# Performance work log

Measured on AMD Instinct MI355X. Metric: run time of the kernel, lower is better.

## Reference

```python
import jax, jax.numpy as jnp
import numpy as np

N = 100000
E = 3200000
IN = 128
HID = 128   # 2 * out_channels
OUT = 64


def setup_inputs() -> dict:
    key = jax.random.key(0)
    ks = jax.random.split(key, 8)
    x = jax.random.normal(ks[0], (N, IN), dtype=jnp.float32)
    edge_index = jax.random.randint(ks[1], (2, E), 0, N, dtype=jnp.int64)
    s1 = 1.0 / np.sqrt(IN)
    s2 = 1.0 / np.sqrt(HID)
    # PyG GraphConv per layer: lin_rel (with bias) applied to aggregated neighbors,
    # lin_root (no bias) applied to the node itself. Linear weight is (out, in).
    W1_rel = jax.random.uniform(ks[2], (HID, IN), jnp.float32, -s1, s1)
    b1 = jax.random.uniform(ks[3], (HID,), jnp.float32, -s1, s1)
    W1_root = jax.random.uniform(ks[4], (HID, IN), jnp.float32, -s1, s1)
    W2_rel = jax.random.uniform(ks[5], (OUT, HID), jnp.float32, -s2, s2)
    b2 = jax.random.uniform(ks[6], (OUT,), jnp.float32, -s2, s2)
    W2_root = jax.random.uniform(ks[7], (OUT, HID), jnp.float32, -s2, s2)
    return {"x": x, "edge_index": edge_index, "W1_rel": W1_rel, "b1": b1,
            "W1_root": W1_root, "W2_rel": W2_rel, "b2": b2, "W2_root": W2_root}


def _graph_conv(h, src, dst, W_rel, b, W_root, num_nodes):
    # sum-aggregate neighbor features at dst, then affine combine with root term
    agg = jax.ops.segment_sum(h[src], dst, num_segments=num_nodes)  # [N, d_in]
    return agg @ W_rel.T + b + h @ W_root.T


def reference(x, edge_index, W1_rel, b1, W1_root, W2_rel, b2, W2_root):
    src = edge_index[0]
    dst = edge_index[1]
    n = x.shape[0]
    h = _graph_conv(x, src, dst, W1_rel, b1, W1_root, n)
    h = jax.nn.relu(h)  # dropout p=0.0 -> identity
    return _graph_conv(h, src, dst, W2_rel, b2, W2_root, n)
```

## Files before the change

kernel.cpp:

```cpp
#include <hip/hip_runtime.h>
#include <hip/hip_bf16.h>


#define EB 8192
#define NB_MAX 512

typedef __attribute__((ext_vector_type(8))) short bf16x8;
typedef __attribute__((ext_vector_type(4))) float f32x4;
typedef __attribute__((ext_vector_type(2))) float f32x2;

__device__ __forceinline__ uint pack_bf16x2(float a, float b) {
    __hip_bfloat162 p = __float22bfloat162_rn(make_float2(a, b));
    return *(uint*)&p;
}

__device__ __forceinline__ uchar pack_fp8(float v) {
    uint p = __builtin_amdgcn_cvt_pk_fp8_f32(v, v, 0, false);
    return (uchar)(p & 0xff);
}

__device__ __forceinline__ float bflo(uint g) { return __uint_as_float(g << 16); }
__device__ __forceinline__ float bfhi(uint g) { return __uint_as_float(g & 0xffff0000u); }


__global__ __launch_bounds__(256) void bucket_hist(const int* __restrict__ dst, int E,
                                                   int NB, int* __restrict__ hist) {
    __shared__ int h[NB_MAX];
    int t = threadIdx.x;
    for (int i = t; i < NB; i += 256) h[i] = 0;
    __syncthreads();
    int e0 = blockIdx.x * EB, e1 = min(E, e0 + EB);
    for (int e = e0 + t; e < e1; e += 256) atomicAdd(&h[dst[e] >> 8], 1);
    __syncthreads();
    int* row = hist + (size_t)blockIdx.x * NB;
    for (int i = t; i < NB; i += 256) row[i] = h[i];
}

__global__ __launch_bounds__(256) void scan_blocks(int* __restrict__ hist, int NBLK,
                                                   int NB, int* __restrict__ total) {
    __shared__ int s[256];
    __shared__ int carry;
    int b = blockIdx.x, t = threadIdx.x;
    if (t == 0) carry = 0;
    __syncthreads();
    for (int start = 0; start < NBLK; start += 256) {
        int i = start + t;
        int v = (i < NBLK) ? hist[(size_t)i * NB + b] : 0;
        s[t] = v;
        __syncthreads();
        for (int off = 1; off < 256; off <<= 1) {
            int u = (t >= off) ? s[t - off] : 0;
            __syncthreads();
            s[t] += u;
            __syncthreads();
        }
        if (i < NBLK) hist[(size_t)i * NB + b] = carry + s[t] - v;
        __syncthreads();
        if (t == 255) carry += s[255];
        __syncthreads();
    }
    if (t == 0) total[b] = carry;
}

__global__ __launch_bounds__(512) void scan_total(const int* __restrict__ total, int NB,
                                                  int* __restrict__ base) {
    __shared__ int s[512];
    int t = threadIdx.x;
    int v = (t < NB) ? total[t] : 0;
    s[t] = v;
    __syncthreads();
    for (int off = 1; off < 512; off <<= 1) {
        int u = (t >= off) ? s[t - off] : 0;
        __syncthreads();
        s[t] += u;
        __syncthreads();
    }
    if (t < NB) base[t] = s[t] - v;
}

__global__ __launch_bounds__(256) void bucket_scatter(const int* __restrict__ src,
                                                      const int* __restrict__ dst, int E,
                                                      int NB, const int* __restrict__ hist,
                                                      const int* __restrict__ base,
                                                      uint* __restrict__ ebuf) {
    __shared__ int cur[NB_MAX];
    int t = threadIdx.x, blk = blockIdx.x;
    const int* row = hist + (size_t)blk * NB;
    for (int i = t; i < NB; i += 256) cur[i] = base[i] + row[i];
    __syncthreads();
    int e0 = blk * EB, e1 = min(E, e0 + EB);
    for (int e = e0 + t; e < e1; e += 256) {
        int d = dst[e];
        int p = atomicAdd(&cur[d >> 8], 1);
        ebuf[p] = ((uint)(d & 255) << 24) | (uint)src[e];
    }
}

__global__ __launch_bounds__(256) void build_csr_bucket(const uint* __restrict__ ebuf,
                                                        const int* __restrict__ base,
                                                        const int* __restrict__ total,
                                                        int NB, int N, int E,
                                                        int* __restrict__ rowptr,
                                                        int* __restrict__ col) {
    __shared__ int cnt[256];
    __shared__ int s[256];
    __shared__ int cur[256];
    int b = blockIdx.x, t = threadIdx.x;
    int e0 = base[b], e1 = e0 + total[b];
    cnt[t] = 0;
    __syncthreads();
    for (int e = e0 + t; e < e1; e += 256) atomicAdd(&cnt[ebuf[e] >> 24], 1);
    __syncthreads();
    int v = cnt[t];
    s[t] = v;
    __syncthreads();
    for (int off = 1; off < 256; off <<= 1) {
        int u = (t >= off) ? s[t - off] : 0;
        __syncthreads();
        s[t] += u;
        __syncthreads();
    }
    int start = e0 + s[t] - v;
    int node = (b << 8) + t;
    if (node < N) rowptr[node] = start;
    if (b == NB - 1 && t == 0) rowptr[N] = E;
    cur[t] = start;
    __syncthreads();
    for (int e = e0 + t; e < e1; e += 256) {
        uint ev = ebuf[e];
        int p = atomicAdd(&cur[ev >> 24], 1);
        col[p] = (int)(ev & 0xFFFFFFu);
    }
}


#define LDK 72

template <int C, bool A_BF16, bool Y_FP8>
__global__ __launch_bounds__(256, 2) void gemm_mfma(const void* __restrict__ Aptr,
                                                    const float* __restrict__ Wa,
                                                    const float* __restrict__ Wb,
                                                    const float* __restrict__ bias,
                                                    void* __restrict__ Yout,
                                                    float* __restrict__ Z, int n_rows) {
    __shared__ ushort Xs[128 * LDK];
    __shared__ ushort Ws[128 * LDK];

    const int t = threadIdx.x;
    const int lane = t & 63;
    const int wave = t >> 6;
    const int wm = wave >> 1, wn = wave & 1;
    const int row0 = blockIdx.x * 128;
    const int tn = blockIdx.y;
    const int fr = lane & 15;
    const int quad = lane >> 4;

    f32x4 acc[4][4];
#pragma unroll
    for (int i = 0; i < 4; i++)
#pragma unroll
        for (int j = 0; j < 4; j++) acc[i][j] = (f32x4){0.f, 0.f, 0.f, 0.f};

    for (int ko = 0; ko < 2; ++ko) {
        if (A_BF16) {
            const ushort* A = (const ushort*)Aptr;
#pragma unroll
            for (int j = 0; j < 4; ++j) {
                int f = j * 256 + t;
                int r = f >> 3, c = f & 7;
                int grow = row0 + r;
                uint4 v = make_uint4(0u, 0u, 0u, 0u);
                if (grow < n_rows)
                    v = *(const uint4*)(A + (size_t)grow * 128 + ko * 64 + c * 8);
                *(uint4*)(&Xs[r * LDK + c * 8]) = v;
            }
        } else {
            const float* A = (const float*)Aptr;
#pragma unroll
            for (int j = 0; j < 8; ++j) {
                int f = j * 256 + t;
                int r = f >> 4, c = f & 15;
                int grow = row0 + r;
                float4 v = make_float4(0.f, 0.f, 0.f, 0.f);
                if (grow < n_rows)
                    v = *(const float4*)(A + (size_t)grow * 128 + ko * 64 + c * 4);
                uint2 u;
                u.x = pack_bf16x2(v.x, v.y);
                u.y = pack_bf16x2(v.z, v.w);
                *(uint2*)(&Xs[r * LDK + c * 4]) = u;
            }
        }
#pragma unroll
        for (int j = 0; j < 8; ++j) {
            int f = j * 256 + t;
            int r = f >> 4, c = f & 15;
            int grow = tn * 128 + r;
            const float* Wr = (grow < C) ? (Wa + (size_t)grow * 128)
                                         : (Wb + (size_t)(grow - C) * 128);
            float4 v = *(const float4*)(Wr + ko * 64 + c * 4);
            uint2 u;
            u.x = pack_bf16x2(v.x, v.y);
            u.y = pack_bf16x2(v.z, v.w);
            *(uint2*)(&Ws[r * LDK + c * 4]) = u;
        }
        __syncthreads();

#pragma unroll
        for (int ks = 0; ks < 2; ++ks) {
            bf16x8 a[4], b[4];
#pragma unroll
            for (int mt = 0; mt < 4; ++mt)
                a[mt] = *(const bf16x8*)(&Xs[(wm * 64 + mt * 16 + fr) * LDK +
                                             ks * 32 + quad * 8]);
#pragma unroll
            for (int nt = 0; nt < 4; ++nt)
                b[nt] = *(const bf16x8*)(&Ws[(wn * 64 + nt * 16 + fr) * LDK +
                                             ks * 32 + quad * 8]);
#pragma unroll
            for (int mt = 0; mt < 4; ++mt)
#pragma unroll
                for (int nt = 0; nt < 4; ++nt)
                    acc[mt][nt] = __builtin_amdgcn_mfma_f32_16x16x32_bf16(
                        a[mt], b[nt], acc[mt][nt], 0, 0, 0);
        }
        __syncthreads();
    }

#pragma unroll
    for (int nt = 0; nt < 4; ++nt) {
        int gcol = tn * 128 + wn * 64 + nt * 16 + fr;
        if (gcol < C) {
#pragma unroll
            for (int mt = 0; mt < 4; ++mt) {
#pragma unroll
                for (int r = 0; r < 4; ++r) {
                    int grow = row0 + wm * 64 + mt * 16 + quad * 4 + r;
                    if (grow < n_rows) {
                        if (Y_FP8) {
                            ((uchar*)Yout)[(size_t)grow * C + gcol] =
                                pack_fp8(acc[mt][nt][r]);
                        } else {
                            __hip_bfloat16 hb = __float2bfloat16(acc[mt][nt][r]);
                            ((ushort*)Yout)[(size_t)grow * C + gcol] = *(ushort*)&hb;
                        }
                    }
                }
            }
        } else {
            float bv = bias[gcol - C];
#pragma unroll
            for (int mt = 0; mt < 4; ++mt) {
#pragma unroll
                for (int r = 0; r < 4; ++r) {
                    int grow = row0 + wm * 64 + mt * 16 + quad * 4 + r;
                    if (grow < n_rows)
                        Z[(size_t)grow * C + (gcol - C)] = acc[mt][nt][r] + bv;
                }
            }
        }
    }
}


__global__ __launch_bounds__(256) void agg_relu_l1(const uchar* __restrict__ Y1,
                                                   const float* __restrict__ Z1,
                                                   const int* __restrict__ rowptr,
                                                   const int* __restrict__ col,
                                                   ushort* __restrict__ h, int n_nodes) {
    int node = (blockIdx.x * 256 + threadIdx.x) >> 6;
    if (node >= n_nodes) return;
    int lane = threadIdx.x & 63;
    int sub = lane >> 3;
    int cg  = lane & 7;
    int beg = rowptr[node], end = rowptr[node + 1];
    float acc[16];
#pragma unroll
    for (int i = 0; i < 16; i++) acc[i] = 0.f;

    int e = beg;
    for (; e + 16 <= end; e += 16) {
        int s0 = col[e + sub];
        int s1 = col[e + 8 + sub];
        uint4 v0 = *(const uint4*)(Y1 + (size_t)s0 * 128 + cg * 16);
        uint4 v1 = *(const uint4*)(Y1 + (size_t)s1 * 128 + cg * 16);
        f32x2 p;
        p = __builtin_amdgcn_cvt_pk_f32_fp8(v0.x, false); acc[0] += p[0]; acc[1] += p[1];
        p = __builtin_amdgcn_cvt_pk_f32_fp8(v0.x, true);  acc[2] += p[0]; acc[3] += p[1];
        p = __builtin_amdgcn_cvt_pk_f32_fp8(v0.y, false); acc[4] += p[0]; acc[5] += p[1];
        p = __builtin_amdgcn_cvt_pk_f32_fp8(v0.y, true);  acc[6] += p[0]; acc[7] += p[1];
        p = __builtin_amdgcn_cvt_pk_f32_fp8(v0.z, false); acc[8] += p[0]; acc[9] += p[1];
        p = __builtin_amdgcn_cvt_pk_f32_fp8(v0.z, true);  acc[10] += p[0]; acc[11] += p[1];
        p = __builtin_amdgcn_cvt_pk_f32_fp8(v0.w, false); acc[12] += p[0]; acc[13] += p[1];
        p = __builtin_amdgcn_cvt_pk_f32_fp8(v0.w, true);  acc[14] += p[0]; acc[15] += p[1];
        p = __builtin_amdgcn_cvt_pk_f32_fp8(v1.x, false); acc[0] += p[0]; acc[1] += p[1];
        p = __builtin_amdgcn_cvt_pk_f32_fp8(v1.x, true);  acc[2] += p[0]; acc[3] += p[1];
        p = __builtin_amdgcn_cvt_pk_f32_fp8(v1.y, false); acc[4] += p[0]; acc[5] += p[1];
        p = __builtin_amdgcn_cvt_pk_f32_fp8(v1.y, true);  acc[6] += p[0]; acc[7] += p[1];
        p = __builtin_amdgcn_cvt_pk_f32_fp8(v1.z, false); acc[8] += p[0]; acc[9] += p[1];
        p = __builtin_amdgcn_cvt_pk_f32_fp8(v1.z, true);  acc[10] += p[0]; acc[11] += p[1];
        p = __builtin_amdgcn_cvt_pk_f32_fp8(v1.w, false); acc[12] += p[0]; acc[13] += p[1];
        p = __builtin_amdgcn_cvt_pk_f32_fp8(v1.w, true);  acc[14] += p[0]; acc[15] += p[1];
    }
    for (; e < end; e += 8) {
        int ee = e + sub;
        uint4 v = make_uint4(0u, 0u, 0u, 0u);
        if (ee < end)
            v = *(const uint4*)(Y1 + (size_t)col[ee] * 128 + cg * 16);
        f32x2 p;
        p = __builtin_amdgcn_cvt_pk_f32_fp8(v.x, false); acc[0] += p[0]; acc[1] += p[1];
        p = __builtin_amdgcn_cvt_pk_f32_fp8(v.x, true);  acc[2] += p[0]; acc[3] += p[1];
        p = __builtin_amdgcn_cvt_pk_f32_fp8(v.y, false); acc[4] += p[0]; acc[5] += p[1];
        p = __builtin_amdgcn_cvt_pk_f32_fp8(v.y, true);  acc[6] += p[0]; acc[7] += p[1];
        p = __builtin_amdgcn_cvt_pk_f32_fp8(v.z, false); acc[8] += p[0]; acc[9] += p[1];
        p = __builtin_amdgcn_cvt_pk_f32_fp8(v.z, true);  acc[10] += p[0]; acc[11] += p[1];
        p = __builtin_amdgcn_cvt_pk_f32_fp8(v.w, false); acc[12] += p[0]; acc[13] += p[1];
        p = __builtin_amdgcn_cvt_pk_f32_fp8(v.w, true);  acc[14] += p[0]; acc[15] += p[1];
    }

#pragma unroll
    for (int off = 8; off < 64; off <<= 1)
#pragma unroll
        for (int i = 0; i < 16; i++) acc[i] += __shfl_xor(acc[i], off, 64);

    if (sub == 0) {
        const float4* zp = (const float4*)(Z1 + (size_t)node * 128 + cg * 16);
        uint o[8];
#pragma unroll
        for (int q = 0; q < 4; ++q) {
            float4 z = zp[q];
            float r0 = acc[q * 4 + 0] + z.x;
            float r1 = acc[q * 4 + 1] + z.y;
            float r2 = acc[q * 4 + 2] + z.z;
            float r3 = acc[q * 4 + 3] + z.w;
            r0 = r0 > 0.f ? r0 : 0.f;
            r1 = r1 > 0.f ? r1 : 0.f;
            r2 = r2 > 0.f ? r2 : 0.f;
            r3 = r3 > 0.f ? r3 : 0.f;
            o[q * 2 + 0] = pack_bf16x2(r0, r1);
            o[q * 2 + 1] = pack_bf16x2(r2, r3);
        }
        uint* hp = (uint*)(h + (size_t)node * 128) + cg * 8;
        *(uint4*)(hp + 0) = make_uint4(o[0], o[1], o[2], o[3]);
        *(uint4*)(hp + 4) = make_uint4(o[4], o[5], o[6], o[7]);
    }
}


__global__ __launch_bounds__(256) void agg_l2(const ushort* __restrict__ Y2,
                                              const float* __restrict__ Z2,
                                              const int* __restrict__ rowptr,
                                              const int* __restrict__ col,
                                              float* __restrict__ out, int n_nodes) {
    int node = (blockIdx.x * 256 + threadIdx.x) >> 6;
    if (node >= n_nodes) return;
    int lane = threadIdx.x & 63;
    int sub = lane >> 3;
    int cg  = lane & 7;
    int beg = rowptr[node], end = rowptr[node + 1];
    float acc[8];
#pragma unroll
    for (int i = 0; i < 8; i++) acc[i] = 0.f;

    int e = beg;
    for (; e + 16 <= end; e += 16) {
        int s0 = col[e + sub];
        int s1 = col[e + 8 + sub];
        uint4 v0 = *(const uint4*)(Y2 + (size_t)s0 * 64 + cg * 8);
        uint4 v1 = *(const uint4*)(Y2 + (size_t)s1 * 64 + cg * 8);
        acc[0] += bflo(v0.x) + bflo(v1.x);
        acc[1] += bfhi(v0.x) + bfhi(v1.x);
        acc[2] += bflo(v0.y) + bflo(v1.y);
        acc[3] += bfhi(v0.y) + bfhi(v1.y);
        acc[4] += bflo(v0.z) + bflo(v1.z);
        acc[5] += bfhi(v0.z) + bfhi(v1.z);
        acc[6] += bflo(v0.w) + bflo(v1.w);
        acc[7] += bfhi(v0.w) + bfhi(v1.w);
    }
    for (; e < end; e += 8) {
        int ee = e + sub;
        uint4 v = make_uint4(0u, 0u, 0u, 0u);
        if (ee < end)
            v = *(const uint4*)(Y2 + (size_t)col[ee] * 64 + cg * 8);
        acc[0] += bflo(v.x);
        acc[1] += bfhi(v.x);
        acc[2] += bflo(v.y);
        acc[3] += bfhi(v.y);
        acc[4] += bflo(v.z);
        acc[5] += bfhi(v.z);
        acc[6] += bflo(v.w);
        acc[7] += bfhi(v.w);
    }

#pragma unroll
    for (int off = 8; off < 64; off <<= 1)
#pragma unroll
        for (int i = 0; i < 8; i++) acc[i] += __shfl_xor(acc[i], off, 64);

    if (sub == 0) {
        const float4* zp = (const float4*)(Z2 + (size_t)node * 64 + cg * 8);
        float4 z0 = zp[0], z1 = zp[1];
        float4 o0 = {acc[0] + z0.x, acc[1] + z0.y, acc[2] + z0.z, acc[3] + z0.w};
        float4 o1 = {acc[4] + z1.x, acc[5] + z1.y, acc[6] + z1.z, acc[7] + z1.w};
        float4* op = (float4*)(out + (size_t)node * 64 + cg * 8);
        op[0] = o0;
        op[1] = o1;
    }
}


extern "C" void kernel_launch(void* const* d_in, const int* in_sizes, int n_in,
                              void* d_out, int out_size, void* d_ws, size_t ws_size,
                              hipStream_t stream) {
    const float* x       = (const float*)d_in[0];
    const int*   ei      = (const int*)d_in[1];
    const float* W1_rel  = (const float*)d_in[2];
    const float* b1      = (const float*)d_in[3];
    const float* W1_root = (const float*)d_in[4];
    const float* W2_rel  = (const float*)d_in[5];
    const float* b2      = (const float*)d_in[6];
    const float* W2_root = (const float*)d_in[7];
    float* out = (float*)d_out;

    const int N = in_sizes[0] / 128;
    const int E = in_sizes[1] / 2;
    const int* srcA = ei;
    const int* dstA = ei + E;
    const int NB   = (N + 255) >> 8;
    const int NBLK = (E + EB - 1) / EB;

    char* ws = (char*)d_ws;
    size_t cur = 0;
    auto alloc = [&](size_t bytes) -> void* {
        size_t o = cur;
        cur = (cur + bytes + 511) & ~(size_t)511;
        return (void*)(ws + o);
    };
    uchar*  Y1  = (uchar*)alloc((size_t)N * 128);
    float*  Z1  = (float*)alloc((size_t)N * 128 * 4);
    ushort* h   = (ushort*)alloc((size_t)N * 128 * 2);
    ushort* Y2  = (ushort*)alloc((size_t)N * 64 * 2);
    float*  Z2  = (float*)alloc((size_t)N * 64 * 4);
    int* rowptr = (int*)alloc((size_t)(N + 1) * 4);
    int* colA   = (int*)alloc((size_t)E * 4);
    int* hist   = (int*)alloc((size_t)NBLK * NB * 4);
    int* btotal = (int*)alloc((size_t)NB_MAX * 4);
    int* bbase  = (int*)alloc((size_t)NB_MAX * 4);
    uint* ebuf  = (uint*)h;

    bucket_hist<<<NBLK, 256, 0, stream>>>(dstA, E, NB, hist);
    scan_blocks<<<NB, 256, 0, stream>>>(hist, NBLK, NB, btotal);
    scan_total<<<1, 512, 0, stream>>>(btotal, NB, bbase);
    bucket_scatter<<<NBLK, 256, 0, stream>>>(srcA, dstA, E, NB, hist, bbase, ebuf);
    build_csr_bucket<<<NB, 256, 0, stream>>>(ebuf, bbase, btotal, NB, N, E, rowptr, colA);

    const int gblk = (N + 127) / 128;
    gemm_mfma<128, false, true><<<dim3(gblk, 2), 256, 0, stream>>>(
        x, W1_rel, W1_root, b1, Y1, Z1, N);
    agg_relu_l1<<<(N + 3) / 4, 256, 0, stream>>>(Y1, Z1, rowptr, colA, h, N);
    gemm_mfma<64, true, false><<<dim3(gblk, 1), 256, 0, stream>>>(
        h, W2_rel, W2_root, b2, Y2, Z2, N);
    agg_l2<<<(N + 3) / 4, 256, 0, stream>>>(Y2, Z2, rowptr, colA, out, N);
}
```

Before: 426.1 us.

## Pre-convert weights to bf16, load GEMM operands directly, unroll gather loops

Adds a small kernel that converts both layers' weights to bf16 once per call. The GEMMs now read their A and B fragments straight from global memory into registers, with no LDS staging or barriers, and occupancy is raised to 3 blocks. The aggregation kernels process 32 edges per iteration and accumulate into packed float2 vectors. Dropping LDS gives up data reuse across waves, so each wave issues more redundant global and L2 loads. The deeper unroll aims for more memory-level parallelism in the gathers.

```diff
diff --git a/kernel.cpp b/kernel.cpp
--- a/kernel.cpp
+++ b/kernel.cpp
@@ -134,18 +134,43 @@
 }
 
 
-#define LDK 72
+__global__ __launch_bounds__(256) void prep_w(const float* __restrict__ W1_rel,
+                                              const float* __restrict__ W1_root,
+                                              const float* __restrict__ W2_rel,
+                                              const float* __restrict__ W2_root,
+                                              ushort* __restrict__ Wb1,
+                                              ushort* __restrict__ Wb2) {
+    int t = blockIdx.x * 256 + threadIdx.x;
+    if (t < 8192) {
+        int idx = t * 4;
+        int row = idx >> 7, c = idx & 127;
+        const float* src = (row < 128) ? W1_rel + (size_t)row * 128 + c
+                                       : W1_root + (size_t)(row - 128) * 128 + c;
+        float4 v = *(const float4*)src;
+        uint2 u;
+        u.x = pack_bf16x2(v.x, v.y);
+        u.y = pack_bf16x2(v.z, v.w);
+        *(uint2*)(Wb1 + idx) = u;
+    } else if (t < 12288) {
+        int idx = (t - 8192) * 4;
+        int row = idx >> 7, c = idx & 127;
+        const float* src = (row < 64) ? W2_rel + (size_t)row * 128 + c
+                                      : W2_root + (size_t)(row - 64) * 128 + c;
+        float4 v = *(const float4*)src;
+        uint2 u;
+        u.x = pack_bf16x2(v.x, v.y);
+        u.y = pack_bf16x2(v.z, v.w);
+        *(uint2*)(Wb2 + idx) = u;
+    }
+}
+
 
 template <int C, bool A_BF16, bool Y_FP8>
-__global__ __launch_bounds__(256, 2) void gemm_mfma(const void* __restrict__ Aptr,
-                                                    const float* __restrict__ Wa,
-                                                    const float* __restrict__ Wb,
-                                                    const float* __restrict__ bias,
-                                                    void* __restrict__ Yout,
-                                                    float* __restrict__ Z, int n_rows) {
-    __shared__ ushort Xs[128 * LDK];
-    __shared__ ushort Ws[128 * LDK];
-
+__global__ __launch_bounds__(256, 3) void gemm_direct(const void* __restrict__ Aptr,
+                                                      const ushort* __restrict__ Wb16,
+                                                      const float* __restrict__ bias,
+                                                      void* __restrict__ Yout,
+                                                      float* __restrict__ Z, int n_rows) {
     const int t = threadIdx.x;
     const int lane = t & 63;
     const int wave = t >> 6;
@@ -161,69 +186,43 @@
 #pragma unroll
         for (int j = 0; j < 4; j++) acc[i][j] = (f32x4){0.f, 0.f, 0.f, 0.f};
 
-    for (int ko = 0; ko < 2; ++ko) {
-        if (A_BF16) {
-            const ushort* A = (const ushort*)Aptr;
-#pragma unroll
-            for (int j = 0; j < 4; ++j) {
-                int f = j * 256 + t;
-                int r = f >> 3, c = f & 7;
-                int grow = row0 + r;
-                uint4 v = make_uint4(0u, 0u, 0u, 0u);
-                if (grow < n_rows)
-                    v = *(const uint4*)(A + (size_t)grow * 128 + ko * 64 + c * 8);
-                *(uint4*)(&Xs[r * LDK + c * 8]) = v;
+    int ar[4];
+#pragma unroll
+    for (int mt = 0; mt < 4; ++mt) {
+        int r = row0 + wm * 64 + mt * 16 + fr;
+        ar[mt] = (r < n_rows) ? r : (n_rows - 1);
+    }
+    const int brbase = tn * 128 + wn * 64;
+
+#pragma unroll
+    for (int kk = 0; kk < 4; ++kk) {
+        const int kb = kk * 32 + quad * 8;
+        bf16x8 a[4], b[4];
+#pragma unroll
+        for (int mt = 0; mt < 4; ++mt) {
+            if (A_BF16) {
+                a[mt] = *(const bf16x8*)((const ushort*)Aptr + (size_t)ar[mt] * 128 + kb);
+            } else {
+                const float* p = (const float*)Aptr + (size_t)ar[mt] * 128 + kb;
+                float4 v0 = *(const float4*)p;
+                float4 v1 = *(const float4*)(p + 4);
+                uint4 u;
+                u.x = pack_bf16x2(v0.x, v0.y);
+                u.y = pack_bf16x2(v0.z, v0.w);
+                u.z = pack_bf16x2(v1.x, v1.y);
+                u.w = pack_bf16x2(v1.z, v1.w);
+                a[mt] = *(bf16x8*)&u;
             }
-        } else {
-            const float* A = (const float*)Aptr;
-#pragma unroll
-            for (int j = 0; j < 8; ++j) {
-                int f = j * 256 + t;
-                int r = f >> 4, c = f & 15;
-                int grow = row0 + r;
-                float4 v = make_float4(0.f, 0.f, 0.f, 0.f);
-                if (grow < n_rows)
-                    v = *(const float4*)(A + (size_t)grow * 128 + ko * 64 + c * 4);
-                uint2 u;
-                u.x = pack_bf16x2(v.x, v.y);
-                u.y = pack_bf16x2(v.z, v.w);
-                *(uint2*)(&Xs[r * LDK + c * 4]) = u;
-            }
-        }
-#pragma unroll
-        for (int j = 0; j < 8; ++j) {
-            int f = j * 256 + t;
-            int r = f >> 4, c = f & 15;
-            int grow = tn * 128 + r;
-            const float* Wr = (grow < C) ? (Wa + (size_t)grow * 128)
-                                         : (Wb + (size_t)(grow - C) * 128);
-            float4 v = *(const float4*)(Wr + ko * 64 + c * 4);
-            uint2 u;
-            u.x = pack_bf16x2(v.x, v.y);
-            u.y = pack_bf16x2(v.z, v.w);
-            *(uint2*)(&Ws[r * LDK + c * 4]) = u;
-        }
-        __syncthreads();
-
-#pragma unroll
-        for (int ks = 0; ks < 2; ++ks) {
-            bf16x8 a[4], b[4];
-#pragma unroll
-            for (int mt = 0; mt < 4; ++mt)
-                a[mt] = *(const bf16x8*)(&Xs[(wm * 64 + mt * 16 + fr) * LDK +
-                                             ks * 32 + quad * 8]);
+        }
+#pragma unroll
+        for (int nt = 0; nt < 4; ++nt)
+            b[nt] = *(const bf16x8*)(Wb16 + (size_t)(brbase + nt * 16 + fr) * 128 + kb);
+#pragma unroll
+        for (int mt = 0; mt < 4; ++mt)
 #pragma unroll
             for (int nt = 0; nt < 4; ++nt)
-                b[nt] = *(const bf16x8*)(&Ws[(wn * 64 + nt * 16 + fr) * LDK +
-                                             ks * 32 + quad * 8]);
-#pragma unroll
-            for (int mt = 0; mt < 4; ++mt)
-#pragma unroll
-                for (int nt = 0; nt < 4; ++nt)
-                    acc[mt][nt] = __builtin_amdgcn_mfma_f32_16x16x32_bf16(
-                        a[mt], b[nt], acc[mt][nt], 0, 0, 0);
-        }
-        __syncthreads();
+                acc[mt][nt] = __builtin_amdgcn_mfma_f32_16x16x32_bf16(
+                    a[mt], b[nt], acc[mt][nt], 0, 0, 0);
     }
 
 #pragma unroll
@@ -262,6 +261,19 @@
 }
 
 
+#define ACC_FP8(v)                                                           \
+    {                                                                        \
+        f32x2 p;                                                             \
+        p = __builtin_amdgcn_cvt_pk_f32_fp8((v).x, false); acc2[0] += p;     \
+        p = __builtin_amdgcn_cvt_pk_f32_fp8((v).x, true);  acc2[1] += p;     \
+        p = __builtin_amdgcn_cvt_pk_f32_fp8((v).y, false); acc2[2] += p;     \
+        p = __builtin_amdgcn_cvt_pk_f32_fp8((v).y, true);  acc2[3] += p;     \
+        p = __builtin_amdgcn_cvt_pk_f32_fp8((v).z, false); acc2[4] += p;     \
+        p = __builtin_amdgcn_cvt_pk_f32_fp8((v).z, true);  acc2[5] += p;     \
+        p = __builtin_amdgcn_cvt_pk_f32_fp8((v).w, false); acc2[6] += p;     \
+        p = __builtin_amdgcn_cvt_pk_f32_fp8((v).w, true);  acc2[7] += p;     \
+    }
+
 __global__ __launch_bounds__(256) void agg_relu_l1(const uchar* __restrict__ Y1,
                                                    const float* __restrict__ Z1,
                                                    const int* __restrict__ rowptr,
@@ -273,54 +285,50 @@
     int sub = lane >> 3;
     int cg  = lane & 7;
     int beg = rowptr[node], end = rowptr[node + 1];
-    float acc[16];
-#pragma unroll
-    for (int i = 0; i < 16; i++) acc[i] = 0.f;
+    f32x2 acc2[8];
+#pragma unroll
+    for (int i = 0; i < 8; i++) acc2[i] = (f32x2){0.f, 0.f};
 
     int e = beg;
+    for (; e + 32 <= end; e += 32) {
+        int s0 = col[e + sub];
+        int s1 = col[e + 8 + sub];
+        int s2 = col[e + 16 + sub];
+        int s3 = col[e + 24 + sub];
+        uint4 v0 = *(const uint4*)(Y1 + (size_t)s0 * 128 + cg * 16);
+        uint4 v1 = *(const uint4*)(Y1 + (size_t)s1 * 128 + cg * 16);
+        uint4 v2 = *(const uint4*)(Y1 + (size_t)s2 * 128 + cg * 16);
+        uint4 v3 = *(const uint4*)(Y1 + (size_t)s3 * 128 + cg * 16);
+        ACC_FP8(v0);
+        ACC_FP8(v1);
+        ACC_FP8(v2);
+        ACC_FP8(v3);
+    }
     for (; e + 16 <= end; e += 16) {
         int s0 = col[e + sub];
         int s1 = col[e + 8 + sub];
         uint4 v0 = *(const uint4*)(Y1 + (size_t)s0 * 128 + cg * 16);
         uint4 v1 = *(const uint4*)(Y1 + (size_t)s1 * 128 + cg * 16);
-        f32x2 p;
-        p = __builtin_amdgcn_cvt_pk_f32_fp8(v0.x, false); acc[0] += p[0]; acc[1] += p[1];
-        p = __builtin_amdgcn_cvt_pk_f32_fp8(v0.x, true);  acc[2] += p[0]; acc[3] += p[1];
-        p = __builtin_amdgcn_cvt_pk_f32_fp8(v0.y, false); acc[4] += p[0]; acc[5] += p[1];
-        p = __builtin_amdgcn_cvt_pk_f32_fp8(v0.y, true);  acc[6] += p[0]; acc[7] += p[1];
-        p = __builtin_amdgcn_cvt_pk_f32_fp8(v0.z, false); acc[8] += p[0]; acc[9] += p[1];
-        p = __builtin_amdgcn_cvt_pk_f32_fp8(v0.z, true);  acc[10] += p[0]; acc[11] += p[1];
-        p = __builtin_amdgcn_cvt_pk_f32_fp8(v0.w, false); acc[12] += p[0]; acc[13] += p[1];
-        p = __builtin_amdgcn_cvt_pk_f32_fp8(v0.w, true);  acc[14] += p[0]; acc[15] += p[1];
-        p = __builtin_amdgcn_cvt_pk_f32_fp8(v1.x, false); acc[0] += p[0]; acc[1] += p[1];
-        p = __builtin_amdgcn_cvt_pk_f32_fp8(v1.x, true);  acc[2] += p[0]; acc[3] += p[1];
-        p = __builtin_amdgcn_cvt_pk_f32_fp8(v1.y, false); acc[4] += p[0]; acc[5] += p[1];
-        p = __builtin_amdgcn_cvt_pk_f32_fp8(v1.y, true);  acc[6] += p[0]; acc[7] += p[1];
-        p = __builtin_amdgcn_cvt_pk_f32_fp8(v1.z, false); acc[8] += p[0]; acc[9] += p[1];
-        p = __builtin_amdgcn_cvt_pk_f32_fp8(v1.z, true);  acc[10] += p[0]; acc[11] += p[1];
-        p = __builtin_amdgcn_cvt_pk_f32_fp8(v1.w, false); acc[12] += p[0]; acc[13] += p[1];
-        p = __builtin_amdgcn_cvt_pk_f32_fp8(v1.w, true);  acc[14] += p[0]; acc[15] += p[1];
+        ACC_FP8(v0);
+        ACC_FP8(v1);
     }
     for (; e < end; e += 8) {
         int ee = e + sub;
         uint4 v = make_uint4(0u, 0u, 0u, 0u);
         if (ee < end)
             v = *(const uint4*)(Y1 + (size_t)col[ee] * 128 + cg * 16);
-        f32x2 p;
-        p = __builtin_amdgcn_cvt_pk_f32_fp8(v.x, false); acc[0] += p[0]; acc[1] += p[1];
-        p = __builtin_amdgcn_cvt_pk_f32_fp8(v.x, true);  acc[2] += p[0]; acc[3] += p[1];
-        p = __builtin_amdgcn_cvt_pk_f32_fp8(v.y, false); acc[4] += p[0]; acc[5] += p[1];
-        p = __builtin_amdgcn_cvt_pk_f32_fp8(v.y, true);  acc[6] += p[0]; acc[7] += p[1];
-        p = __builtin_amdgcn_cvt_pk_f32_fp8(v.z, false); acc[8] += p[0]; acc[9] += p[1];
-        p = __builtin_amdgcn_cvt_pk_f32_fp8(v.z, true);  acc[10] += p[0]; acc[11] += p[1];
-        p = __builtin_amdgcn_cvt_pk_f32_fp8(v.w, false); acc[12] += p[0]; acc[13] += p[1];
-        p = __builtin_amdgcn_cvt_pk_f32_fp8(v.w, true);  acc[14] += p[0]; acc[15] += p[1];
+        ACC_FP8(v);
     }
 
 #pragma unroll
     for (int off = 8; off < 64; off <<= 1)
 #pragma unroll
-        for (int i = 0; i < 16; i++) acc[i] += __shfl_xor(acc[i], off, 64);
+        for (int i = 0; i < 8; i++) {
+            f32x2 o;
+            o[0] = __shfl_xor(acc2[i][0], off, 64);
+            o[1] = __shfl_xor(acc2[i][1], off, 64);
+            acc2[i] += o;
+        }
 
     if (sub == 0) {
         const float4* zp = (const float4*)(Z1 + (size_t)node * 128 + cg * 16);
@@ -328,10 +336,10 @@
 #pragma unroll
         for (int q = 0; q < 4; ++q) {
             float4 z = zp[q];
-            float r0 = acc[q * 4 + 0] + z.x;
-            float r1 = acc[q * 4 + 1] + z.y;
-            float r2 = acc[q * 4 + 2] + z.z;
-            float r3 = acc[q * 4 + 3] + z.w;
+            float r0 = acc2[q * 2 + 0][0] + z.x;
+            float r1 = acc2[q * 2 + 0][1] + z.y;
+            float r2 = acc2[q * 2 + 1][0] + z.z;
+            float r3 = acc2[q * 2 + 1][1] + z.w;
             r0 = r0 > 0.f ? r0 : 0.f;
             r1 = r1 > 0.f ? r1 : 0.f;
             r2 = r2 > 0.f ? r2 : 0.f;
@@ -345,6 +353,14 @@
     }
 }
 
+
+#define ACC_BF16(v)                                       \
+    {                                                     \
+        acc2[0] += (f32x2){bflo((v).x), bfhi((v).x)};     \
+        acc2[1] += (f32x2){bflo((v).y), bfhi((v).y)};     \
+        acc2[2] += (f32x2){bflo((v).z), bfhi((v).z)};     \
+        acc2[3] += (f32x2){bflo((v).w), bfhi((v).w)};     \
+    }
 
 __global__ __launch_bounds__(256) void agg_l2(const ushort* __restrict__ Y2,
                                               const float* __restrict__ Z2,
@@ -357,50 +373,58 @@
     int sub = lane >> 3;
     int cg  = lane & 7;
     int beg = rowptr[node], end = rowptr[node + 1];
-    float acc[8];
-#pragma unroll
-    for (int i = 0; i < 8; i++) acc[i] = 0.f;
+    f32x2 acc2[4];
+#pragma unroll
+    for (int i = 0; i < 4; i++) acc2[i] = (f32x2){0.f, 0.f};
 
     int e = beg;
+    for (; e + 32 <= end; e += 32) {
+        int s0 = col[e + sub];
+        int s1 = col[e + 8 + sub];
+        int s2 = col[e + 16 + sub];
+        int s3 = col[e + 24 + sub];
+        uint4 v0 = *(const uint4*)(Y2 + (size_t)s0 * 64 + cg * 8);
+        uint4 v1 = *(const uint4*)(Y2 + (size_t)s1 * 64 + cg * 8);
+        uint4 v2 = *(const uint4*)(Y2 + (size_t)s2 * 64 + cg * 8);
+        uint4 v3 = *(const uint4*)(Y2 + (size_t)s3 * 64 + cg * 8);
+        ACC_BF16(v0);
+        ACC_BF16(v1);
+        ACC_BF16(v2);
+        ACC_BF16(v3);
+    }
     for (; e + 16 <= end; e += 16) {
         int s0 = col[e + sub];
         int s1 = col[e + 8 + sub];
         uint4 v0 = *(const uint4*)(Y2 + (size_t)s0 * 64 + cg * 8);
         uint4 v1 = *(const uint4*)(Y2 + (size_t)s1 * 64 + cg * 8);
-        acc[0] += bflo(v0.x) + bflo(v1.x);
-        acc[1] += bfhi(v0.x) + bfhi(v1.x);
-        acc[2] += bflo(v0.y) + bflo(v1.y);
-        acc[3] += bfhi(v0.y) + bfhi(v1.y);
-        acc[4] += bflo(v0.z) + bflo(v1.z);
-        acc[5] += bfhi(v0.z) + bfhi(v1.z);
-        acc[6] += bflo(v0.w) + bflo(v1.w);
-        acc[7] += bfhi(v0.w) + bfhi(v1.w);
+        ACC_BF16(v0);
+        ACC_BF16(v1);
     }
     for (; e < end; e += 8) {
         int ee = e + sub;
         uint4 v = make_uint4(0u, 0u, 0u, 0u);
         if (ee < end)
             v = *(const uint4*)(Y2 + (size_t)col[ee] * 64 + cg * 8);
-        acc[0] += bflo(v.x);
-        acc[1] += bfhi(v.x);
-        acc[2] += bflo(v.y);
-        acc[3] += bfhi(v.y);
-        acc[4] += bflo(v.z);
-        acc[5] += bfhi(v.z);
-        acc[6] += bflo(v.w);
-        acc[7] += bfhi(v.w);
+        ACC_BF16(v);
     }
 
 #pragma unroll
     for (int off = 8; off < 64; off <<= 1)
 #pragma unroll
-        for (int i = 0; i < 8; i++) acc[i] += __shfl_xor(acc[i], off, 64);
+        for (int i = 0; i < 4; i++) {
+            f32x2 o;
+            o[0] = __shfl_xor(acc2[i][0], off, 64);
+            o[1] = __shfl_xor(acc2[i][1], off, 64);
+            acc2[i] += o;
+        }
 
     if (sub == 0) {
         const float4* zp = (const float4*)(Z2 + (size_t)node * 64 + cg * 8);
         float4 z0 = zp[0], z1 = zp[1];
-        float4 o0 = {acc[0] + z0.x, acc[1] + z0.y, acc[2] + z0.z, acc[3] + z0.w};
-        float4 o1 = {acc[4] + z1.x, acc[5] + z1.y, acc[6] + z1.z, acc[7] + z1.w};
+        float4 o0 = {acc2[0][0] + z0.x, acc2[0][1] + z0.y,
+                     acc2[1][0] + z0.z, acc2[1][1] + z0.w};
+        float4 o1 = {acc2[2][0] + z1.x, acc2[2][1] + z1.y,
+                     acc2[3][0] + z1.z, acc2[3][1] + z1.w};
         float4* op = (float4*)(out + (size_t)node * 64 + cg * 8);
         op[0] = o0;
         op[1] = o1;
@@ -445,7 +469,11 @@
     int* hist   = (int*)alloc((size_t)NBLK * NB * 4);
     int* btotal = (int*)alloc((size_t)NB_MAX * 4);
     int* bbase  = (int*)alloc((size_t)NB_MAX * 4);
+    ushort* Wb1 = (ushort*)alloc((size_t)256 * 128 * 2);
+    ushort* Wb2 = (ushort*)alloc((size_t)128 * 128 * 2);
     uint* ebuf  = (uint*)h;
+
+    prep_w<<<48, 256, 0, stream>>>(W1_rel, W1_root, W2_rel, W2_root, Wb1, Wb2);
 
     bucket_hist<<<NBLK, 256, 0, stream>>>(dstA, E, NB, hist);
     scan_blocks<<<NB, 256, 0, stream>>>(hist, NBLK, NB, btotal);
@@ -454,10 +482,10 @@
     build_csr_bucket<<<NB, 256, 0, stream>>>(ebuf, bbase, btotal, NB, N, E, rowptr, colA);
 
     const int gblk = (N + 127) / 128;
-    gemm_mfma<128, false, true><<<dim3(gblk, 2), 256, 0, stream>>>(
-        x, W1_rel, W1_root, b1, Y1, Z1, N);
+    gemm_direct<128, false, true><<<dim3(gblk, 2), 256, 0, stream>>>(
+        x, Wb1, b1, Y1, Z1, N);
     agg_relu_l1<<<(N + 3) / 4, 256, 0, stream>>>(Y1, Z1, rowptr, colA, h, N);
-    gemm_mfma<64, true, false><<<dim3(gblk, 1), 256, 0, stream>>>(
-        h, W2_rel, W2_root, b2, Y2, Z2, N);
+    gemm_direct<64, true, false><<<dim3(gblk, 1), 256, 0, stream>>>(
+        h, Wb2, b2, Y2, Z2, N);
     agg_l2<<<(N + 3) / 4, 256, 0, stream>>>(Y2, Z2, rowptr, colA, out, N);
 }
```

Result: no change. 426.8 us (+0.2%).
